# Performance work log

Hardware: AMD Instinct MI355X
Metric: run time of the kernel (lower is better)

## Reference

```python
import jax, jax.numpy as jnp
import numpy as np

B, N, DIN, DOUT = 16, 256, 64, 64
TEMP = 2.0          # temperatures[0]
POOL_K = 0.5        # pool_ratios[0]
BN_EPS = 1e-5


def setup_inputs() -> dict:
    key = jax.random.key(0)
    ks = jax.random.split(key, 8)
    g = lambda i, shape: (jax.random.normal(ks[i], shape, jnp.float32) * 0.08)
    return {
        "x": jax.random.normal(ks[0], (B, N, DIN), jnp.float32),
        # GraphAttentionLayer params
        "W_att": g(1, (DIN, DOUT)), "b_att": jnp.zeros((DOUT,), jnp.float32),
        "att_w": g(2, (DOUT,)),                      # att_weight [DOUT,1] squeezed
        "W_pwa": g(3, (DIN, DOUT)), "b_pwa": jnp.zeros((DOUT,), jnp.float32),
        "W_pna": g(4, (DIN, DOUT)), "b_pna": jnp.zeros((DOUT,), jnp.float32),
        "bn_scale": jnp.ones((DOUT,), jnp.float32),
        "bn_bias": jnp.zeros((DOUT,), jnp.float32),
        # GraphPool params
        "pool_w": g(5, (DOUT,)), "pool_b": jnp.zeros((), jnp.float32),
    }


def reference(x, W_att, b_att, att_w, W_pwa, b_pwa, W_pna, b_pna,
              bn_scale, bn_bias, pool_w, pool_b):
    # --- GraphAttentionLayer (eval mode: dropout = identity) ---
    # pairwise node multiplication: [B, i, j, DIN]
    pm = x[:, :, None, :] * x[:, None, :, :]
    att = jnp.tanh(jnp.einsum('bijd,de->bije', pm, W_att) + b_att)   # [B,N,N,DOUT]
    logits = jnp.einsum('bije,e->bij', att, att_w) / TEMP            # [B,N,N]
    # torch softmax over dim=-2 of [B,i,j,1] == axis j (the aggregated axis)
    A = jax.nn.softmax(logits, axis=2)                               # [B,N,N]
    agg = jnp.einsum('bij,bjd->bid', A, x)                           # [B,N,DIN]
    h = (agg @ W_pwa + b_pwa) + (x @ W_pna + b_pna)                  # [B,N,DOUT]
    # BatchNorm1d eval with running_mean=0, running_var=1
    h = h * (bn_scale / jnp.sqrt(1.0 + BN_EPS)) + bn_bias
    h = jax.nn.selu(h)
    # --- GraphPool (eval mode: dropout = identity) ---
    scores = jax.nn.sigmoid(h @ pool_w + pool_b)                     # [B,N]
    k = max(int(N * POOL_K), 1)
    _, idx = jax.lax.top_k(scores, k)                                # [B,k]
    hw = h * scores[:, :, None]
    out = jnp.take_along_axis(hw, idx[:, :, None], axis=1)           # [B,k,DOUT]
    return out
```

## Files before the change

### kernel.cpp

```cpp
#include <hip/hip_runtime.h>
#include <hip/hip_bf16.h>
#include <math.h>

#define BB 16
#define NN 256
#define DD 64
#define KTOP 128

typedef short s16x8 __attribute__((ext_vector_type(8)));
typedef float f32x4 __attribute__((ext_vector_type(4)));

typedef union { s16x8 v; unsigned u[4]; } frag_u;
typedef union { __hip_bfloat162 b2; unsigned u; } cvu;

__device__ __forceinline__ float asf(unsigned u){ union{unsigned u;float f;}c; c.u=u; return c.f; }

__device__ __forceinline__ void split2(float v0, float v1, unsigned& hu, unsigned& lu) {
    cvu c; c.b2 = __float22bfloat162_rn(make_float2(v0, v1));
    unsigned h = c.u;
    float l0 = v0 - asf(h << 16);
    float l1 = v1 - asf(h & 0xffff0000u);
    c.b2 = __float22bfloat162_rn(make_float2(l0, l1));
    hu = h; lu = c.u;
}

__global__ __launch_bounds__(512, 4) void k_fused(
    const float* __restrict__ x, const float* __restrict__ W_att,
    const float* __restrict__ b_att, const float* __restrict__ att_w,
    const float* __restrict__ Wpwa, const float* __restrict__ bpwa,
    const float* __restrict__ Wpna, const float* __restrict__ bpna,
    const float* __restrict__ bnsc, const float* __restrict__ bnbi,
    const float* __restrict__ poolw, const float* __restrict__ poolb,
    float* __restrict__ hbuf, float* __restrict__ scores)
{
    const int ig = blockIdx.x;
    const int b  = blockIdx.y;
    const int tid = threadIdx.x;
    const int w = tid >> 6, lane = tid & 63;
    const int quad = lane >> 4, c16 = lane & 15;
    const int jb = w * 32;
    const int ibase = ig * 4;

    __shared__ s16x8 sB[2][4][2][64];
    __shared__ float sXi[4 * 64];
    __shared__ float sL[4][256];
    __shared__ float sAgg[4][64];

    if (tid < 256) sXi[tid] = x[(b * NN + ibase + (tid >> 6)) * DD + (tid & 63)];

    const float L2E2 = 2.8853900817779268f;
    float bawL[4], aww[4];
    #pragma unroll
    for (int et = 0; et < 4; ++et) {
        bawL[et] = b_att[et * 16 + c16] * L2E2;
        aww[et]  = att_w[et * 16 + c16];
    }
    float halfS;
    {
        float sa = aww[0] + aww[1] + aww[2] + aww[3];
        sa += __shfl_xor(sa, 1); sa += __shfl_xor(sa, 2);
        sa += __shfl_xor(sa, 4); sa += __shfl_xor(sa, 8);
        halfS = 0.5f * sa;
    }

    frag_u Ah[2][2], Al[2][2];
    #pragma unroll
    for (int jt = 0; jt < 2; ++jt) {
        #pragma unroll
        for (int ks = 0; ks < 2; ++ks) {
            const float* xr = &x[(b * NN + jb + jt * 16 + c16) * DD + ks * 32 + quad * 8];
            float4 a0 = *(const float4*)xr;
            float4 a1 = *(const float4*)(xr + 4);
            split2(a0.x, a0.y, Ah[jt][ks].u[0], Al[jt][ks].u[0]);
            split2(a0.z, a0.w, Ah[jt][ks].u[1], Al[jt][ks].u[1]);
            split2(a1.x, a1.y, Ah[jt][ks].u[2], Al[jt][ks].u[2]);
            split2(a1.z, a1.w, Ah[jt][ks].u[3], Al[jt][ks].u[3]);
        }
    }
    __syncthreads();

    const int bks = w >> 2, bet = w & 3;
    for (int ii = 0; ii < 4; ++ii) {
        {
            const float* xr = &sXi[ii * 64 + bks * 32 + quad * 8];
            float4 c0 = *(const float4*)xr;
            float4 c1 = *(const float4*)(xr + 4);
            float xiv[8] = {c0.x,c0.y,c0.z,c0.w,c1.x,c1.y,c1.z,c1.w};
            const float* wp = &W_att[(bks * 32 + quad * 8) * 64 + bet * 16 + c16];
            float wv[8];
            #pragma unroll
            for (int t = 0; t < 8; ++t) wv[t] = wp[t * 64];
            frag_u bh, bl;
            split2(wv[0] * xiv[0], wv[1] * xiv[1], bh.u[0], bl.u[0]);
            split2(wv[2] * xiv[2], wv[3] * xiv[3], bh.u[1], bl.u[1]);
            split2(wv[4] * xiv[4], wv[5] * xiv[5], bh.u[2], bl.u[2]);
            split2(wv[6] * xiv[6], wv[7] * xiv[7], bh.u[3], bl.u[3]);
            sB[bks][bet][0][lane] = bh.v;
            sB[bks][bet][1][lane] = bl.v;
        }
        __syncthreads();

        float p[2][4];
        #pragma unroll
        for (int jt = 0; jt < 2; ++jt)
            #pragma unroll
            for (int r = 0; r < 4; ++r) p[jt][r] = 0.0f;

        #pragma unroll
        for (int eth = 0; eth < 2; ++eth) {
            f32x4 acc[2][2];
            #pragma unroll
            for (int jt = 0; jt < 2; ++jt)
                #pragma unroll
                for (int e2 = 0; e2 < 2; ++e2)
                    acc[jt][e2] = (f32x4){0.f, 0.f, 0.f, 0.f};

            #pragma unroll
            for (int ks = 0; ks < 2; ++ks) {
                #pragma unroll
                for (int e2 = 0; e2 < 2; ++e2) {
                    const int et = eth * 2 + e2;
                    s16x8 bh = sB[ks][et][0][lane];
                    s16x8 bl = sB[ks][et][1][lane];
                    #pragma unroll
                    for (int jt = 0; jt < 2; ++jt) {
                        acc[jt][e2] = __builtin_amdgcn_mfma_f32_16x16x32_bf16(Ah[jt][ks].v, bh, acc[jt][e2], 0, 0, 0);
                        acc[jt][e2] = __builtin_amdgcn_mfma_f32_16x16x32_bf16(Al[jt][ks].v, bh, acc[jt][e2], 0, 0, 0);
                        acc[jt][e2] = __builtin_amdgcn_mfma_f32_16x16x32_bf16(Ah[jt][ks].v, bl, acc[jt][e2], 0, 0, 0);
                    }
                }
            }

            #pragma unroll
            for (int e2 = 0; e2 < 2; ++e2) {
                const int et = eth * 2 + e2;
                #pragma unroll
                for (int jt = 0; jt < 2; ++jt) {
                    #pragma unroll
                    for (int r = 0; r < 4; ++r) {
                        float arg = fmaf(acc[jt][e2][r], L2E2, bawL[et]);
                        float m = __builtin_amdgcn_exp2f(arg);
                        float rc = __builtin_amdgcn_rcpf(m + 1.0f);
                        p[jt][r] = fmaf(aww[et], rc, p[jt][r]);
                    }
                }
            }
        }

        #pragma unroll
        for (int jt = 0; jt < 2; ++jt) {
            #pragma unroll
            for (int r = 0; r < 4; ++r) {
                float s = p[jt][r];
                s += __shfl_xor(s, 1);
                s += __shfl_xor(s, 2);
                s += __shfl_xor(s, 4);
                s += __shfl_xor(s, 8);
                if (c16 == 0) sL[ii][jb + jt * 16 + quad * 4 + r] = halfS - s;
            }
        }
        __syncthreads();
    }

    if (w < 4) {
        const int i = ibase + w;
        float* row = sL[w];
        float lg0 = row[lane], lg1 = row[lane + 64], lg2 = row[lane + 128], lg3 = row[lane + 192];
        float m = fmaxf(fmaxf(lg0, lg1), fmaxf(lg2, lg3));
        #pragma unroll
        for (int off = 32; off; off >>= 1) m = fmaxf(m, __shfl_xor(m, off));
        float e0 = __expf(lg0 - m), e1 = __expf(lg1 - m), e2 = __expf(lg2 - m), e3 = __expf(lg3 - m);
        float ssum = e0 + e1 + e2 + e3;
        #pragma unroll
        for (int off = 32; off; off >>= 1) ssum += __shfl_xor(ssum, off);
        float inv = 1.0f / ssum;
        row[lane] = e0 * inv; row[lane + 64] = e1 * inv;
        row[lane + 128] = e2 * inv; row[lane + 192] = e3 * inv;
        __asm__ volatile("s_waitcnt lgkmcnt(0)" ::: "memory");

        float agg = 0.0f;
        const float4* A4 = (const float4*)row;
        const float* xb = &x[(b * NN) * DD];
        #pragma unroll 8
        for (int jq = 0; jq < 64; ++jq) {
            float4 a = A4[jq];
            int j = jq * 4;
            agg = fmaf(a.x, xb[(j + 0) * DD + lane], agg);
            agg = fmaf(a.y, xb[(j + 1) * DD + lane], agg);
            agg = fmaf(a.z, xb[(j + 2) * DD + lane], agg);
            agg = fmaf(a.w, xb[(j + 3) * DD + lane], agg);
        }
        sAgg[w][lane] = agg;
        __asm__ volatile("s_waitcnt lgkmcnt(0)" ::: "memory");

        double hacc = (double)bpwa[lane] + (double)bpna[lane];
        #pragma unroll 4
        for (int d = 0; d < 64; ++d) {
            hacc += (double)sAgg[w][d] * (double)Wpwa[d * DD + lane]
                  + (double)sXi[w * 64 + d] * (double)Wpna[d * DD + lane];
        }
        const double bnmul = 0.99999500003749968750e0;
        double hb = hacc * ((double)bnsc[lane] * bnmul) + (double)bnbi[lane];
        float hf = (float)hb;
        const float LAM = 1.0507009873554805f, ALP = 1.6732632423543772f;
        float hs = hf > 0.0f ? LAM * hf : LAM * ALP * (__expf(hf) - 1.0f);
        hbuf[((b * NN) + i) * DD + lane] = hs;

        double z = (double)hs * (double)poolw[lane];
        #pragma unroll
        for (int off = 32; off; off >>= 1) z += __shfl_xor(z, off);
        if (lane == 0) {
            double zz = z + (double)poolb[0];
            scores[b * NN + i] = (float)(1.0 / (1.0 + exp(-zz)));
        }
    }
}

__global__ __launch_bounds__(256) void k_topk(
    const float* __restrict__ scores, const float* __restrict__ hbuf,
    float* __restrict__ out)
{
    const int b = blockIdx.x;
    const int t = threadIdx.x;
    __shared__ float ss[256];
    __shared__ int   perm[KTOP];
    ss[t] = scores[b * NN + t];
    __syncthreads();
    const float my = ss[t];
    int rank = 0;
    #pragma unroll 8
    for (int j = 0; j < 256; ++j) {
        float v = ss[j];
        rank += (v > my) || (v == my && j < t);
    }
    if (rank < KTOP) perm[rank] = t;
    __syncthreads();
    #pragma unroll
    for (int m = t; m < KTOP * DD; m += 256) {
        int r = m >> 6, e = m & 63;
        int i = perm[r];
        out[(b * KTOP + r) * DD + e] = hbuf[((b * NN) + i) * DD + e] * ss[i];
    }
}

extern "C" void kernel_launch(void* const* d_in, const int* in_sizes, int n_in,
                              void* d_out, int out_size, void* d_ws, size_t ws_size,
                              hipStream_t stream) {
    const float* x        = (const float*)d_in[0];
    const float* W_att    = (const float*)d_in[1];
    const float* b_att    = (const float*)d_in[2];
    const float* att_w    = (const float*)d_in[3];
    const float* W_pwa    = (const float*)d_in[4];
    const float* b_pwa    = (const float*)d_in[5];
    const float* W_pna    = (const float*)d_in[6];
    const float* b_pna    = (const float*)d_in[7];
    const float* bn_scale = (const float*)d_in[8];
    const float* bn_bias  = (const float*)d_in[9];
    const float* pool_w   = (const float*)d_in[10];
    const float* pool_b   = (const float*)d_in[11];

    float* hbuf    = (float*)d_ws;
    float* scoresW = hbuf + BB * NN * DD;
    float* out     = (float*)d_out;

    k_fused<<<dim3(64, BB), 512, 0, stream>>>(x, W_att, b_att, att_w,
                                              W_pwa, b_pwa, W_pna, b_pna,
                                              bn_scale, bn_bias, pool_w, pool_b,
                                              hbuf, scoresW);
    k_topk<<<dim3(BB), 256, 0, stream>>>(scoresW, hbuf, out);
}
```

Measured before the change: 138.8 us.

## Double-buffer B fragments, hoist W_att loads, and split top-k gather across blocks

The W_att weight loads move out of the per-row loop, so each thread loads them once. The shared B-fragment buffer is double-buffered so that building the next row's fragments overlaps the current MFMA pass, which drops one barrier per iteration. The top-k kernel now runs on 8×16 blocks, each gathering 16 output rows, where before 16 blocks each gathered 128. Each block recomputes the full rank scan, and the extra shared buffer and held weight registers may raise register and LDS pressure.

```diff
diff --git a/kernel.cpp b/kernel.cpp
--- a/kernel.cpp
+++ b/kernel.cpp
@@ -41,7 +41,7 @@
     const int jb = w * 32;
     const int ibase = ig * 4;
 
-    __shared__ s16x8 sB[2][4][2][64];
+    __shared__ s16x8 sB[2][2][4][2][64];
     __shared__ float sXi[4 * 64];
     __shared__ float sL[4][256];
     __shared__ float sAgg[4][64];
@@ -61,6 +61,14 @@
         sa += __shfl_xor(sa, 1); sa += __shfl_xor(sa, 2);
         sa += __shfl_xor(sa, 4); sa += __shfl_xor(sa, 8);
         halfS = 0.5f * sa;
+    }
+
+    const int bks = w >> 2, bet = w & 3;
+    float wv[8];
+    {
+        const float* wp = &W_att[(bks * 32 + quad * 8) * 64 + bet * 16 + c16];
+        #pragma unroll
+        for (int t = 0; t < 8; ++t) wv[t] = wp[t * 64];
     }
 
     frag_u Ah[2][2], Al[2][2];
@@ -79,27 +87,39 @@
     }
     __syncthreads();
 
-    const int bks = w >> 2, bet = w & 3;
+    {
+        const float* xr = &sXi[0 * 64 + bks * 32 + quad * 8];
+        float4 c0 = *(const float4*)xr;
+        float4 c1 = *(const float4*)(xr + 4);
+        float xiv[8] = {c0.x,c0.y,c0.z,c0.w,c1.x,c1.y,c1.z,c1.w};
+        frag_u bh, bl;
+        split2(wv[0] * xiv[0], wv[1] * xiv[1], bh.u[0], bl.u[0]);
+        split2(wv[2] * xiv[2], wv[3] * xiv[3], bh.u[1], bl.u[1]);
+        split2(wv[4] * xiv[4], wv[5] * xiv[5], bh.u[2], bl.u[2]);
+        split2(wv[6] * xiv[6], wv[7] * xiv[7], bh.u[3], bl.u[3]);
+        sB[0][bks][bet][0][lane] = bh.v;
+        sB[0][bks][bet][1][lane] = bl.v;
+    }
+
+    #pragma unroll
     for (int ii = 0; ii < 4; ++ii) {
-        {
-            const float* xr = &sXi[ii * 64 + bks * 32 + quad * 8];
+        __syncthreads();
+
+        if (ii < 3) {
+            const float* xr = &sXi[(ii + 1) * 64 + bks * 32 + quad * 8];
             float4 c0 = *(const float4*)xr;
             float4 c1 = *(const float4*)(xr + 4);
             float xiv[8] = {c0.x,c0.y,c0.z,c0.w,c1.x,c1.y,c1.z,c1.w};
-            const float* wp = &W_att[(bks * 32 + quad * 8) * 64 + bet * 16 + c16];
-            float wv[8];
-            #pragma unroll
-            for (int t = 0; t < 8; ++t) wv[t] = wp[t * 64];
             frag_u bh, bl;
             split2(wv[0] * xiv[0], wv[1] * xiv[1], bh.u[0], bl.u[0]);
             split2(wv[2] * xiv[2], wv[3] * xiv[3], bh.u[1], bl.u[1]);
             split2(wv[4] * xiv[4], wv[5] * xiv[5], bh.u[2], bl.u[2]);
             split2(wv[6] * xiv[6], wv[7] * xiv[7], bh.u[3], bl.u[3]);
-            sB[bks][bet][0][lane] = bh.v;
-            sB[bks][bet][1][lane] = bl.v;
-        }
-        __syncthreads();
-
+            sB[(ii + 1) & 1][bks][bet][0][lane] = bh.v;
+            sB[(ii + 1) & 1][bks][bet][1][lane] = bl.v;
+        }
+
+        const int cur = ii & 1;
         float p[2][4];
         #pragma unroll
         for (int jt = 0; jt < 2; ++jt)
@@ -120,8 +140,8 @@
                 #pragma unroll
                 for (int e2 = 0; e2 < 2; ++e2) {
                     const int et = eth * 2 + e2;
-                    s16x8 bh = sB[ks][et][0][lane];
-                    s16x8 bl = sB[ks][et][1][lane];
+                    s16x8 bh = sB[cur][ks][et][0][lane];
+                    s16x8 bl = sB[cur][ks][et][1][lane];
                     #pragma unroll
                     for (int jt = 0; jt < 2; ++jt) {
                         acc[jt][e2] = __builtin_amdgcn_mfma_f32_16x16x32_bf16(Ah[jt][ks].v, bh, acc[jt][e2], 0, 0, 0);
@@ -159,8 +179,8 @@
                 if (c16 == 0) sL[ii][jb + jt * 16 + quad * 4 + r] = halfS - s;
             }
         }
-        __syncthreads();
-    }
+    }
+    __syncthreads();
 
     if (w < 4) {
         const int i = ibase + w;
@@ -220,10 +240,11 @@
     const float* __restrict__ scores, const float* __restrict__ hbuf,
     float* __restrict__ out)
 {
-    const int b = blockIdx.x;
+    const int c = blockIdx.x;
+    const int b = blockIdx.y;
     const int t = threadIdx.x;
     __shared__ float ss[256];
-    __shared__ int   perm[KTOP];
+    __shared__ int   perm[16];
     ss[t] = scores[b * NN + t];
     __syncthreads();
     const float my = ss[t];
@@ -233,13 +254,13 @@
         float v = ss[j];
         rank += (v > my) || (v == my && j < t);
     }
-    if (rank < KTOP) perm[rank] = t;
-    __syncthreads();
-    #pragma unroll
-    for (int m = t; m < KTOP * DD; m += 256) {
+    if ((rank >> 4) == c) perm[rank & 15] = t;
+    __syncthreads();
+    #pragma unroll
+    for (int m = t; m < 16 * DD; m += 256) {
         int r = m >> 6, e = m & 63;
         int i = perm[r];
-        out[(b * KTOP + r) * DD + e] = hbuf[((b * NN) + i) * DD + e] * ss[i];
+        out[(b * KTOP + c * 16 + r) * DD + e] = hbuf[((b * NN) + i) * DD + e] * ss[i];
     }
 }
 
@@ -267,5 +288,5 @@
                                               W_pwa, b_pwa, W_pna, b_pna,
                                               bn_scale, bn_bias, pool_w, pool_b,
                                               hbuf, scoresW);
-    k_topk<<<dim3(BB), 256, 0, stream>>>(scoresW, hbuf, out);
-}
+    k_topk<<<dim3(8, BB), 256, 0, stream>>>(scoresW, hbuf, out);
+}
```

New measurement: 136.4 us. No clear change (-1.7%).
